# Performance work log

Measured on AMD Instinct MI355X. Metric: run time of the kernel, lower is better.

The kernel has to match this reference:

```python
import jax, jax.numpy as jnp
import numpy as np

B, S, D, H = 2, 2048, 1024, 16
DK = D // H  # 64, per-head key/value dim


def setup_inputs() -> dict:
    key = jax.random.key(0)
    ks = jax.random.split(key, 8)
    q = jax.random.normal(ks[0], (B, S, D), dtype=jnp.float32)
    k = jax.random.normal(ks[1], (B, S, D), dtype=jnp.float32)
    v = jax.random.normal(ks[2], (B, S, D), dtype=jnp.float32)
    # per-head projection weights, initialized like torch.randn in the original
    W_q = jax.random.normal(ks[3], (H, D, DK), dtype=jnp.float32)
    W_k = jax.random.normal(ks[4], (H, D, DK), dtype=jnp.float32)
    W_v = jax.random.normal(ks[5], (H, D, DK), dtype=jnp.float32)
    # output nn.Linear(H*DK, D): weight [D, H*DK], bias [D]
    bound = 1.0 / np.sqrt(H * DK)
    W_o = jax.random.uniform(ks[6], (D, H * DK), dtype=jnp.float32, minval=-bound, maxval=bound)
    b_o = jax.random.uniform(ks[7], (D,), dtype=jnp.float32, minval=-bound, maxval=bound)
    return {"q": q, "k": k, "v": v, "W_q": W_q, "W_k": W_k, "W_v": W_v, "W_o": W_o, "b_o": b_o}


def reference(q, k, v, W_q, W_k, W_v, W_o, b_o):
    dk = W_q.shape[-1]
    # batched per-head projections (replaces the Python loop over heads)
    qh = jnp.einsum('bsd,hdk->bhsk', q, W_q)  # [B,H,S,DK]
    kh = jnp.einsum('bsd,hdk->bhsk', k, W_k)
    vh = jnp.einsum('bsd,hdk->bhsk', v, W_v)
    scale = jnp.asarray(np.sqrt(dk), qh.dtype)
    scores = jnp.einsum('bhsk,bhtk->bhst', qh, kh) / scale  # [B,H,S,S]
    attn = jax.nn.softmax(scores, axis=-1)
    ctx = jnp.einsum('bhst,bhtk->bhsk', attn, vh)  # [B,H,S,DK]
    # concat heads along feature dim (matches torch.cat(..., dim=2))
    b, h, s, d = ctx.shape
    ctx = ctx.transpose(0, 2, 1, 3).reshape(b, s, h * d)  # [B,S,H*DK]
    return ctx @ W_o.T + b_o  # [B,S,D]
```

## Files before the change

kernel.cpp:

```cpp
#include <hip/hip_runtime.h>
#include <math.h>

#define B_ 2
#define S_ 2048
#define D_ 1024
#define H_ 16
#define ATTN_C 0.18033688011f

typedef unsigned short ushort_t;
typedef __attribute__((ext_vector_type(8))) short short8;
typedef __attribute__((ext_vector_type(4))) short short4v;
typedef __attribute__((ext_vector_type(4))) float f32x4;
typedef __attribute__((ext_vector_type(2))) float f32x2;
typedef __attribute__((ext_vector_type(16))) float f32x16;
typedef __attribute__((ext_vector_type(4))) unsigned int uint4v;

#define MFMA(A, B, C) __builtin_amdgcn_mfma_f32_32x32x16_bf16((A), (B), (C), 0, 0, 0)
#define Z16 {0.f,0.f,0.f,0.f,0.f,0.f,0.f,0.f,0.f,0.f,0.f,0.f,0.f,0.f,0.f,0.f}

__device__ __forceinline__ ushort_t bf16rn(float x) {
    unsigned int u = __builtin_bit_cast(unsigned int, x);
    u += 0x7FFFu + ((u >> 16) & 1u);
    return (ushort_t)(u >> 16);
}
__device__ __forceinline__ float bf16tof(ushort_t h) {
    return __builtin_bit_cast(float, (unsigned int)h << 16);
}
__device__ __forceinline__ unsigned cvtpk(float lo, float hi) {
    unsigned r;
    asm("v_cvt_pk_bf16_f32 %0, %1, %2" : "=v"(r) : "v"(lo), "v"(hi));
    return r;
}
__device__ __forceinline__ void gload16(const void* g, void* l) {
    __builtin_amdgcn_global_load_lds(
        (const __attribute__((address_space(1))) unsigned int*)(unsigned long long)g,
        (__attribute__((address_space(3))) unsigned int*)(unsigned int)(unsigned long long)l,
        16, 0, 0);
}

__global__ __launch_bounds__(256) void cvtx_kernel(
    const float* __restrict__ Xq, const float* __restrict__ Xk,
    const float* __restrict__ Xv,
    ushort_t* __restrict__ Xh, ushort_t* __restrict__ Xl)
{
    const int pr = blockIdx.y;
    const float* X = pr == 0 ? Xq : pr == 1 ? Xk : Xv;
    const size_t idx = ((size_t)blockIdx.x * 256 + threadIdx.x) * 8;
    f32x4 v0 = *(const f32x4*)(X + idx);
    f32x4 v1 = *(const f32x4*)(X + idx + 4);
    float f[8] = {v0.x, v0.y, v0.z, v0.w, v1.x, v1.y, v1.z, v1.w};
    short8 hi, lo;
#pragma unroll
    for (int i = 0; i < 8; ++i) {
        ushort_t hh = bf16rn(f[i]);
        hi[i] = (short)hh;
        lo[i] = (short)bf16rn(f[i] - bf16tof(hh));
    }
    const size_t base = (size_t)pr * 2 * S_ * D_;
    *(short8*)(Xh + base + idx) = hi;
    if (pr < 2) *(short8*)(Xl + base + idx) = lo;
}

__global__ __launch_bounds__(256) void cvtw_kernel(
    const float* __restrict__ Wq, const float* __restrict__ Wk,
    const float* __restrict__ Wv,
    ushort_t* __restrict__ wqh, ushort_t* __restrict__ wql,
    ushort_t* __restrict__ wkh, ushort_t* __restrict__ wkl,
    ushort_t* __restrict__ wvh)
{
    __shared__ float T[64][68];
    const int dt = blockIdx.x, h = blockIdx.y, mat = blockIdx.z;
    const int tid = threadIdx.x;
    const float* W = mat == 0 ? Wq : mat == 1 ? Wk : Wv;
    const float* Wb = W + ((size_t)h * 1024 + dt * 64) * 64;
#pragma unroll
    for (int u = 0; u < 4; ++u) {
        int idx = tid + u * 256;
        int d = idx >> 4, c4 = idx & 15;
        f32x4 v = *(const f32x4*)(Wb + (size_t)d * 64 + c4 * 4);
        T[d][c4 * 4 + 0] = v.x; T[d][c4 * 4 + 1] = v.y;
        T[d][c4 * 4 + 2] = v.z; T[d][c4 * 4 + 3] = v.w;
    }
    __syncthreads();
    ushort_t* oh = mat == 0 ? wqh : mat == 1 ? wkh : wvh;
    ushort_t* ol = mat == 0 ? wql : mat == 1 ? wkl : nullptr;
#pragma unroll
    for (int u = 0; u < 4; ++u) {
        int idx = tid + u * 256;
        int n = idx >> 4, c4 = idx & 15;
        float v0 = T[c4 * 4 + 0][n], v1 = T[c4 * 4 + 1][n];
        float v2 = T[c4 * 4 + 2][n], v3 = T[c4 * 4 + 3][n];
        ushort_t h0 = bf16rn(v0), h1 = bf16rn(v1), h2 = bf16rn(v2), h3 = bf16rn(v3);
        size_t off = ((size_t)h * 64 + n) * 1024 + dt * 64 + c4 * 4;
        short4v hv = {(short)h0, (short)h1, (short)h2, (short)h3};
        *(short4v*)(oh + off) = hv;
        if (ol) {
            short4v lv = {(short)bf16rn(v0 - bf16tof(h0)), (short)bf16rn(v1 - bf16tof(h1)),
                          (short)bf16rn(v2 - bf16tof(h2)), (short)bf16rn(v3 - bf16tof(h3))};
            *(short4v*)(ol + off) = lv;
        }
    }
}

__global__ __launch_bounds__(256) void cvtwo_kernel(
    const float* __restrict__ Wo, ushort_t* __restrict__ wob)
{
    size_t idx = (size_t)blockIdx.x * 256 + threadIdx.x;
    f32x4 v = *(const f32x4*)(Wo + idx * 4);
    short4v o = {(short)bf16rn(v.x), (short)bf16rn(v.y),
                 (short)bf16rn(v.z), (short)bf16rn(v.w)};
    *(short4v*)(wob + idx * 4) = o;
}

__global__ __launch_bounds__(256, 2) void proj_kernel(
    const ushort_t* __restrict__ Xh, const ushort_t* __restrict__ Xl,
    const ushort_t* __restrict__ Wh_q, const ushort_t* __restrict__ Wl_q,
    const ushort_t* __restrict__ Wh_k, const ushort_t* __restrict__ Wl_k,
    const ushort_t* __restrict__ Wh_v,
    ushort_t* __restrict__ Oq_h, ushort_t* __restrict__ Oq_l,
    ushort_t* __restrict__ Ok_h, ushort_t* __restrict__ Ok_l,
    ushort_t* __restrict__ Ovt)
{
    __shared__ __align__(16) ushort_t Xs[128 * 128];
    __shared__ __align__(16) ushort_t Ws[128 * 128];
    const int tid = threadIdx.x;
    const int wv = tid >> 6, lane = tid & 63;
    const int lo32 = lane & 31, g = lane >> 5;
    const int wm = wv >> 1, wn = wv & 1;
    const int lrow = lane >> 4, lg = lane & 15;
    const int m0 = blockIdx.x * 128;
    const int n0 = blockIdx.y * 128;
    const int pr = blockIdx.z >> 1, b = blockIdx.z & 1;
    const bool split = (pr != 2);
    const ushort_t* Whp = pr == 0 ? Wh_q : pr == 1 ? Wh_k : Wh_v;
    const ushort_t* Wlp = pr == 0 ? Wl_q : pr == 1 ? Wl_k : Wh_v;
    const ushort_t* Xhb = Xh + ((size_t)(pr * 2 + b) * S_ + m0) * D_;
    const ushort_t* Xlb = Xl + ((size_t)(pr * 2 + b) * S_ + m0) * D_;
    f32x16 a00 = Z16, a01 = Z16, a10 = Z16, a11 = Z16;

    for (int d0 = 0; d0 < D_; d0 += 64) {
        __syncthreads();
#pragma unroll
        for (int u = 0; u < 8; ++u) {
            int row = u * 16 + wv * 4 + lrow;
            int gs = lg ^ (row & 15);
            int half = gs >> 3, c8 = gs & 7;
            const ushort_t* srcX = ((half && split) ? Xlb : Xhb) + (size_t)row * D_ + d0 + c8 * 8;
            gload16(srcX, (char*)Xs + (u * 16 + wv * 4) * 256);
            const ushort_t* srcW = ((half && split) ? Wlp : Whp) + (size_t)(n0 + row) * 1024 + d0 + c8 * 8;
            gload16(srcW, (char*)Ws + (u * 16 + wv * 4) * 256);
        }
        __syncthreads();
#pragma unroll
        for (int ks = 0; ks < 4; ++ks) {
            int coff = ks * 16 + g * 8;
            int r0 = wm * 64 + lo32, r1 = r0 + 32;
            int c0 = wn * 64 + lo32, c1 = c0 + 32;
            short8 a0h = *(const short8*)&Xs[(r0 * 128 + coff) ^ ((r0 & 15) << 3)];
            short8 a1h = *(const short8*)&Xs[(r1 * 128 + coff) ^ ((r1 & 15) << 3)];
            short8 b0h = *(const short8*)&Ws[(c0 * 128 + coff) ^ ((c0 & 15) << 3)];
            short8 b1h = *(const short8*)&Ws[(c1 * 128 + coff) ^ ((c1 & 15) << 3)];
            a00 = MFMA(a0h, b0h, a00);
            a01 = MFMA(a0h, b1h, a01);
            a10 = MFMA(a1h, b0h, a10);
            a11 = MFMA(a1h, b1h, a11);
            if (split) {
                short8 a0l = *(const short8*)&Xs[(r0 * 128 + 64 + coff) ^ ((r0 & 15) << 3)];
                short8 a1l = *(const short8*)&Xs[(r1 * 128 + 64 + coff) ^ ((r1 & 15) << 3)];
                short8 b0l = *(const short8*)&Ws[(c0 * 128 + 64 + coff) ^ ((c0 & 15) << 3)];
                short8 b1l = *(const short8*)&Ws[(c1 * 128 + 64 + coff) ^ ((c1 & 15) << 3)];
                a00 = MFMA(a0h, b0l, a00); a00 = MFMA(a0l, b0h, a00);
                a01 = MFMA(a0h, b1l, a01); a01 = MFMA(a0l, b1h, a01);
                a10 = MFMA(a1h, b0l, a10); a10 = MFMA(a1l, b0h, a10);
                a11 = MFMA(a1h, b1l, a11); a11 = MFMA(a1l, b1h, a11);
            }
        }
    }
    ushort_t* OH = pr == 0 ? Oq_h : pr == 1 ? Ok_h : Ovt;
    ushort_t* OL = pr == 0 ? Oq_l : pr == 1 ? Ok_l : Ovt;
    const bool qscale = (pr == 0);
#define PROJ_STORE(ACC, MT, NT)                                               \
    _Pragma("unroll")                                                         \
    for (int r = 0; r < 16; ++r) {                                            \
        int s_loc = m0 + wm * 64 + (MT) * 32 + (r & 3) + 8 * (r >> 2) + 4 * g;\
        int col = n0 + wn * 64 + (NT) * 32 + lo32;                            \
        int hh_ = col >> 6, nn = col & 63;                                    \
        float val = ACC[r];                                                   \
        if (qscale) val *= ATTN_C;                                            \
        if (split) {                                                          \
            size_t off = (((size_t)b * H_ + hh_) * S_ + s_loc) * 64 + nn;     \
            ushort_t hv = bf16rn(val);                                        \
            OH[off] = hv;                                                     \
            OL[off] = bf16rn(val - bf16tof(hv));                              \
        } else {                                                              \
            size_t offt = (((size_t)b * H_ + hh_) * 64 + nn) * S_ + s_loc;    \
            OH[offt] = bf16rn(val);                                           \
        }                                                                     \
    }
    PROJ_STORE(a00, 0, 0)
    PROJ_STORE(a01, 0, 1)
    PROJ_STORE(a10, 1, 0)
    PROJ_STORE(a11, 1, 1)
#undef PROJ_STORE
}

__global__ __launch_bounds__(256, 2) void attn_kernel(
    const ushort_t* __restrict__ qh_h, const ushort_t* __restrict__ qh_l,
    const ushort_t* __restrict__ kh_h, const ushort_t* __restrict__ kh_l,
    const ushort_t* __restrict__ vt, ushort_t* __restrict__ Opart,
    float* __restrict__ Ml)
{
    __shared__ __align__(16) char smem[32768];
    ushort_t* Vt = (ushort_t*)smem;
    const int tid = threadIdx.x;
    const int wv = tid >> 6, lane = tid & 63;
    const int lo32 = lane & 31, g = lane >> 5;
    const int lrow = lane >> 4, lg = lane & 15;
    const int s0 = blockIdx.x * 256;
    const int h = blockIdx.y;
    const int b = blockIdx.z >> 1, sp = blockIdx.z & 1;
    const size_t bhs = ((size_t)b * H_ + h) * S_ * 64;

    short8 qfh[2][4], qfl[2][4];
#pragma unroll
    for (int c = 0; c < 2; ++c) {
        const ushort_t* Qrh = qh_h + bhs + (size_t)(s0 + wv * 64 + c * 32 + lo32) * 64;
        const ushort_t* Qrl = qh_l + bhs + (size_t)(s0 + wv * 64 + c * 32 + lo32) * 64;
#pragma unroll
        for (int ks = 0; ks < 4; ++ks) {
            qfh[c][ks] = *(const short8*)(Qrh + ks * 16 + g * 8);
            qfl[c][ks] = *(const short8*)(Qrl + ks * 16 + g * 8);
        }
    }
    const ushort_t* Kgh = kh_h + bhs;
    const ushort_t* Kgl = kh_l + bhs;
    const ushort_t* Vtg = vt + ((size_t)b * H_ + h) * 64 * S_;

    f32x16 o00 = Z16, o01 = Z16, o10 = Z16, o11 = Z16;
    float mrun0 = -3.0e38f, mrun1 = -3.0e38f;
    float lrun0 = 0.f, lrun1 = 0.f;
    const int kvbeg = sp * (S_ / 2);

#define MAX16(ST) fmaxf(fmaxf(fmaxf(fmaxf(ST[0], ST[1]), fmaxf(ST[2], ST[3])),   \
                              fmaxf(fmaxf(ST[4], ST[5]), fmaxf(ST[6], ST[7]))),  \
                        fmaxf(fmaxf(fmaxf(ST[8], ST[9]), fmaxf(ST[10], ST[11])), \
                              fmaxf(fmaxf(ST[12], ST[13]), fmaxf(ST[14], ST[15]))))

#define SOFTMAX_PV(ST, MR, LR, OA, OB)                                        \
    {                                                                         \
        float cme = MAX16(ST);                                                \
        cme = fmaxf(cme, __shfl_xor(cme, 32));                                \
        if (!__all(cme <= MR)) {                                              \
            float mnew = fmaxf(MR, cme);                                      \
            float corr = __builtin_amdgcn_exp2f(MR - mnew);                   \
            LR *= corr;                                                       \
            _Pragma("unroll")                                                 \
            for (int r = 0; r < 16; ++r) { OA[r] *= corr; OB[r] *= corr; }    \
            MR = mnew;                                                        \
        }                                                                     \
        float p[16], ls = 0.f;                                                \
        _Pragma("unroll")                                                     \
        for (int r = 0; r < 16; ++r) {                                        \
            p[r] = __builtin_amdgcn_exp2f(ST[r] - MR);                        \
            ls += p[r];                                                       \
        }                                                                     \
        LR += ls;                                                             \
        {                                                                     \
            unsigned w0 = cvtpk(p[0], p[1]), w1 = cvtpk(p[2], p[3]);          \
            unsigned w2 = cvtpk(p[4], p[5]), w3 = cvtpk(p[6], p[7]);          \
            asm("v_permlane32_swap_b32 %0, %1" : "+v"(w0), "+v"(w2));         \
            asm("v_permlane32_swap_b32 %0, %1" : "+v"(w1), "+v"(w3));         \
            uint4v pa = {w0, w1, w2, w3};                                     \
            short8 pf = __builtin_bit_cast(short8, pa);                       \
            OA = MFMA(vfa0, pf, OA);                                          \
            OB = MFMA(vfa1, pf, OB);                                          \
            w0 = cvtpk(p[8], p[9]);  w1 = cvtpk(p[10], p[11]);                \
            w2 = cvtpk(p[12], p[13]); w3 = cvtpk(p[14], p[15]);               \
            asm("v_permlane32_swap_b32 %0, %1" : "+v"(w0), "+v"(w2));         \
            asm("v_permlane32_swap_b32 %0, %1" : "+v"(w1), "+v"(w3));         \
            uint4v pb = {w0, w1, w2, w3};                                     \
            short8 pf2 = __builtin_bit_cast(short8, pb);                      \
            OA = MFMA(vfb0, pf2, OA);                                         \
            OB = MFMA(vfb1, pf2, OB);                                         \
        }                                                                     \
    }

#define LOADK(CI, DST)                                                        \
    {                                                                         \
        int cc = (CI) > 31 ? 31 : (CI);                                       \
        const ushort_t* pn = Kgh + (size_t)(kvbeg + cc * 32 + lo32) * 64 + g * 8; \
        DST[0] = *(const short8*)(pn);                                        \
        DST[1] = *(const short8*)(pn + 16);                                   \
        DST[2] = *(const short8*)(pn + 32);                                   \
        DST[3] = *(const short8*)(pn + 48);                                   \
    }

#define CHUNK_BODY(KC, KN, CI)                                                \
    {                                                                         \
        LOADK((CI) + 1, KN);                                                  \
        f32x16 st0 = Z16, st1 = Z16;                                          \
        st0 = MFMA(KC[0], qfh[0][0], st0);  st1 = MFMA(KC[0], qfh[1][0], st1);\
        st0 = MFMA(KC[1], qfh[0][1], st0);  st1 = MFMA(KC[1], qfh[1][1], st1);\
        st0 = MFMA(KC[2], qfh[0][2], st0);  st1 = MFMA(KC[2], qfh[1][2], st1);\
        st0 = MFMA(KC[3], qfh[0][3], st0);  st1 = MFMA(KC[3], qfh[1][3], st1);\
        float cm0 = MAX16(st0);                                               \
        float cm1 = MAX16(st1);                                               \
        cm0 = fmaxf(cm0, __shfl_xor(cm0, 32));                                \
        cm1 = fmaxf(cm1, __shfl_xor(cm1, 32));                                \
        const bool need0 = !__all(cm0 <= mrun0 - 150.f);                      \
        const bool need1 = !__all(cm1 <= mrun1 - 150.f);                      \
        if (need0 | need1) {                                                  \
            const ushort_t* pl = Kgl + (size_t)(kvbeg + (CI) * 32 + lo32) * 64 + g * 8; \
            short8 kl0 = *(const short8*)(pl);                                \
            short8 kl1 = *(const short8*)(pl + 16);                           \
            short8 kl2 = *(const short8*)(pl + 32);                           \
            short8 kl3 = *(const short8*)(pl + 48);                           \
            if (need0) {                                                      \
                st0 = MFMA(KC[0], qfl[0][0], st0); st0 = MFMA(KC[1], qfl[0][1], st0); \
                st0 = MFMA(KC[2], qfl[0][2], st0); st0 = MFMA(KC[3], qfl[0][3], st0); \
            }                                                                 \
            if (need1) {                                                      \
                st1 = MFMA(KC[0], qfl[1][0], st1); st1 = MFMA(KC[1], qfl[1][1], st1); \
                st1 = MFMA(KC[2], qfl[1][2], st1); st1 = MFMA(KC[3], qfl[1][3], st1); \
            }                                                                 \
            if (need0) {                                                      \
                st0 = MFMA(kl0, qfh[0][0], st0); st0 = MFMA(kl1, qfh[0][1], st0); \
                st0 = MFMA(kl2, qfh[0][2], st0); st0 = MFMA(kl3, qfh[0][3], st0); \
            }                                                                 \
            if (need1) {                                                      \
                st1 = MFMA(kl0, qfh[1][0], st1); st1 = MFMA(kl1, qfh[1][1], st1); \
                st1 = MFMA(kl2, qfh[1][2], st1); st1 = MFMA(kl3, qfh[1][3], st1); \
            }                                                                 \
            const int kvb = ((CI) & 3) * 32;                                  \
            const int vsw = (lo32 & 7) << 3;                                  \
            short8 vfa0 = *(const short8*)&Vt[(lo32 * 128 + kvb + g * 8) ^ vsw];        \
            short8 vfa1 = *(const short8*)&Vt[((lo32 + 32) * 128 + kvb + g * 8) ^ vsw]; \
            short8 vfb0 = *(const short8*)&Vt[(lo32 * 128 + kvb + 16 + g * 8) ^ vsw];   \
            short8 vfb1 = *(const short8*)&Vt[((lo32 + 32) * 128 + kvb + 16 + g * 8) ^ vsw]; \
            if (need0) SOFTMAX_PV(st0, mrun0, lrun0, o00, o01)                \
            if (need1) SOFTMAX_PV(st1, mrun1, lrun1, o10, o11)                \
        }                                                                     \
    }

    short8 kx[4], ky[4];
    LOADK(0, kx);
    int c = 0;
    for (int t = 0; t < 8; ++t) {
        const int kv0 = kvbeg + t * 128;
        __syncthreads();
#pragma unroll
        for (int u = 0; u < 4; ++u) {
            int d = u * 16 + wv * 4 + lrow;
            int gsrc = (lg & 8) | ((lg & 7) ^ (d & 7));
            const ushort_t* src = Vtg + (size_t)d * S_ + kv0 + gsrc * 8;
            gload16(src, (char*)Vt + (u * 16 + wv * 4) * 256);
        }
        __syncthreads();
        CHUNK_BODY(kx, ky, c + 0)
        CHUNK_BODY(ky, kx, c + 1)
        CHUNK_BODY(kx, ky, c + 2)
        CHUNK_BODY(ky, kx, c + 3)
        c += 4;
    }
#undef CHUNK_BODY
#undef LOADK
#undef SOFTMAX_PV
#undef MAX16

    lrun0 += __shfl_xor(lrun0, 32);
    lrun1 += __shfl_xor(lrun1, 32);
    __syncthreads();
    float* Oe = ((float*)smem) + wv * 2048;
    const size_t orowb = (size_t)sp * (B_ * H_ * S_) + ((size_t)b * H_ + h) * S_ + s0 + wv * 64;
#pragma unroll
    for (int r = 0; r < 16; ++r) {
        int dd = (r & 3) + 8 * (r >> 2) + 4 * g;
        int qsw = (lo32 & 7) << 2;
        Oe[(lo32 * 64 + dd) ^ qsw] = o00[r];
        Oe[(lo32 * 64 + 32 + dd) ^ qsw] = o01[r];
    }
#pragma unroll
    for (int rep = 0; rep < 8; ++rep) {
        int idx = lane + rep * 64;
        int qq = idx >> 4, d4 = idx & 15;
        f32x4 ov = *(const f32x4*)&Oe[(qq * 64 + d4 * 4) ^ ((qq & 7) << 2)];
        short4v pk4 = {(short)bf16rn(ov.x), (short)bf16rn(ov.y),
                       (short)bf16rn(ov.z), (short)bf16rn(ov.w)};
        *(short4v*)(Opart + (orowb + qq) * 64 + d4 * 4) = pk4;
    }
    if (g == 0) {
        f32x2 ml = {mrun0, lrun0};
        *(f32x2*)(Ml + (orowb + lo32) * 2) = ml;
    }
    __builtin_amdgcn_s_waitcnt(0);
#pragma unroll
    for (int r = 0; r < 16; ++r) {
        int dd = (r & 3) + 8 * (r >> 2) + 4 * g;
        int qsw = (lo32 & 7) << 2;
        Oe[(lo32 * 64 + dd) ^ qsw] = o10[r];
        Oe[(lo32 * 64 + 32 + dd) ^ qsw] = o11[r];
    }
#pragma unroll
    for (int rep = 0; rep < 8; ++rep) {
        int idx = lane + rep * 64;
        int qq = idx >> 4, d4 = idx & 15;
        f32x4 ov = *(const f32x4*)&Oe[(qq * 64 + d4 * 4) ^ ((qq & 7) << 2)];
        short4v pk4 = {(short)bf16rn(ov.x), (short)bf16rn(ov.y),
                       (short)bf16rn(ov.z), (short)bf16rn(ov.w)};
        *(short4v*)(Opart + (orowb + 32 + qq) * 64 + d4 * 4) = pk4;
    }
    if (g == 0) {
        f32x2 ml = {mrun1, lrun1};
        *(f32x2*)(Ml + (orowb + 32 + lo32) * 2) = ml;
    }
}

__global__ __launch_bounds__(256) void merge_kernel(
    const ushort_t* __restrict__ Opart, const float* __restrict__ Ml,
    ushort_t* __restrict__ ctxb)
{
    const int NROW = B_ * H_ * S_;
    int gidx = blockIdx.x * 256 + threadIdx.x;
    int row = gidx >> 3, d8 = (gidx & 7) * 8;
    f32x2 ml0 = *(const f32x2*)(Ml + (size_t)row * 2);
    f32x2 ml1 = *(const f32x2*)(Ml + ((size_t)NROW + row) * 2);
    float M = fmaxf(ml0.x, ml1.x);
    float w0 = __builtin_amdgcn_exp2f(ml0.x - M);
    float w1 = __builtin_amdgcn_exp2f(ml1.x - M);
    float inv = 1.f / (ml0.y * w0 + ml1.y * w1);
    w0 *= inv; w1 *= inv;
    short8 a = *(const short8*)(Opart + (size_t)row * 64 + d8);
    short8 c = *(const short8*)(Opart + ((size_t)NROW + row) * 64 + d8);
    short8 o;
#pragma unroll
    for (int i = 0; i < 8; ++i) {
        float f = bf16tof((ushort_t)a[i]) * w0 + bf16tof((ushort_t)c[i]) * w1;
        o[i] = (short)bf16rn(f);
    }
    int bb = row >> 15, hh = (row >> 11) & 15, s = row & 2047;
    *(short8*)(ctxb + ((size_t)bb * S_ + s) * D_ + hh * 64 + d8) = o;
}

__global__ __launch_bounds__(128, 2) void outproj_kernel(
    const ushort_t* __restrict__ ctxb, const ushort_t* __restrict__ wob,
    const float* __restrict__ bo, float* __restrict__ Out)
{
    __shared__ __align__(16) ushort_t Cs[128 * 128];
    __shared__ __align__(16) ushort_t Ws2[64 * 128];
    const int tid = threadIdx.x;
    const int wv = tid >> 6, lane = tid & 63;
    const int lo32 = lane & 31, g = lane >> 5;
    const int lrow = lane >> 4, lg = lane & 15;
    const int n0 = blockIdx.x * 64;
    const int m0 = blockIdx.y * 128;
    f32x16 a00 = Z16, a01 = Z16, a10 = Z16, a11 = Z16;
    for (int k0 = 0; k0 < D_; k0 += 128) {
        __syncthreads();
#pragma unroll
        for (int u = 0; u < 16; ++u) {
            int row = u * 8 + wv * 4 + lrow;
            int gs = lg ^ (row & 15);
            const ushort_t* src = ctxb + (size_t)(m0 + row) * D_ + k0 + gs * 8;
            gload16(src, (char*)Cs + (u * 8 + wv * 4) * 256);
        }
#pragma unroll
        for (int u = 0; u < 8; ++u) {
            int row = u * 8 + wv * 4 + lrow;
            int gs = lg ^ (row & 15);
            const ushort_t* src = wob + (size_t)(n0 + row) * D_ + k0 + gs * 8;
            gload16(src, (char*)Ws2 + (u * 8 + wv * 4) * 256);
        }
        __syncthreads();
#pragma unroll
        for (int ks = 0; ks < 8; ++ks) {
            int coff = ks * 16 + g * 8;
            int r0 = wv * 64 + lo32, r1 = r0 + 32;
            int n1 = lo32 + 32;
            short8 A0 = *(const short8*)&Cs[(r0 * 128 + coff) ^ ((r0 & 15) << 3)];
            short8 A1 = *(const short8*)&Cs[(r1 * 128 + coff) ^ ((r1 & 15) << 3)];
            short8 B0 = *(const short8*)&Ws2[(lo32 * 128 + coff) ^ ((lo32 & 15) << 3)];
            short8 B1 = *(const short8*)&Ws2[(n1 * 128 + coff) ^ ((n1 & 15) << 3)];
            a00 = MFMA(A0, B0, a00);
            a01 = MFMA(A0, B1, a01);
            a10 = MFMA(A1, B0, a10);
            a11 = MFMA(A1, B1, a11);
        }
    }
    float b0v = bo[n0 + lo32], b1v = bo[n0 + 32 + lo32];
#define OUT_STORE(ACC, MT, NT, BV)                                          \
    _Pragma("unroll")                                                       \
    for (int r = 0; r < 16; ++r) {                                          \
        int m = m0 + wv * 64 + (MT) * 32 + (r & 3) + 8 * (r >> 2) + 4 * g;  \
        int n = n0 + (NT) * 32 + lo32;                                      \
        Out[(size_t)m * D_ + n] = ACC[r] + (BV);                            \
    }
    OUT_STORE(a00, 0, 0, b0v)
    OUT_STORE(a01, 0, 1, b1v)
    OUT_STORE(a10, 1, 0, b0v)
    OUT_STORE(a11, 1, 1, b1v)
#undef OUT_STORE
}

extern "C" void kernel_launch(void* const* d_in, const int* in_sizes, int n_in,
                              void* d_out, int out_size, void* d_ws,
                              size_t ws_size, hipStream_t stream)
{
    const float* q = (const float*)d_in[0];
    const float* k = (const float*)d_in[1];
    const float* v = (const float*)d_in[2];
    const float* W_q = (const float*)d_in[3];
    const float* W_k = (const float*)d_in[4];
    const float* W_v = (const float*)d_in[5];
    const float* W_o = (const float*)d_in[6];
    const float* b_o = (const float*)d_in[7];
    float* out = (float*)d_out;

    ushort_t* wqt_h = (ushort_t*)d_ws;
    ushort_t* wqt_l = wqt_h + (1 << 20);
    ushort_t* wkt_h = wqt_l + (1 << 20);
    ushort_t* wkt_l = wkt_h + (1 << 20);
    ushort_t* wvt_h = wkt_l + (1 << 20);
    ushort_t* wob   = wvt_h + (1 << 20);
    ushort_t* qh_h  = wob + (1 << 20);
    ushort_t* qh_l  = qh_h + (1 << 22);
    ushort_t* kh_h  = qh_l + (1 << 22);
    ushort_t* kh_l  = kh_h + (1 << 22);
    ushort_t* vtp   = kh_l + (1 << 22);
    ushort_t* Xh    = vtp + (1 << 22);
    ushort_t* Xl    = Xh + 3 * (1 << 22);
    ushort_t* ctxb  = Xh;
    ushort_t* Opart = Xl;
    float*    Ml    = (float*)(Xl + 2 * (size_t)(B_ * H_ * S_) * 64);

    cvtx_kernel<<<dim3(2048, 3), 256, 0, stream>>>(q, k, v, Xh, Xl);
    cvtw_kernel<<<dim3(16, 16, 3), 256, 0, stream>>>(
        W_q, W_k, W_v, wqt_h, wqt_l, wkt_h, wkt_l, wvt_h);
    cvtwo_kernel<<<1024, 256, 0, stream>>>(W_o, wob);
    proj_kernel<<<dim3(16, 8, 6), 256, 0, stream>>>(
        Xh, Xl, wqt_h, wqt_l, wkt_h, wkt_l, wvt_h,
        qh_h, qh_l, kh_h, kh_l, vtp);
    attn_kernel<<<dim3(8, 16, 4), 256, 0, stream>>>(
        qh_h, qh_l, kh_h, kh_l, vtp, Opart, Ml);
    merge_kernel<<<2048, 256, 0, stream>>>(Opart, Ml, ctxb);
    outproj_kernel<<<dim3(16, 32), 128, 0, stream>>>(ctxb, wob, b_o, out);
}
```

Measured before the change: 232.9 us.

## Always compute split-bf16 QK scores with prefetched K low part and larger V tiles

The attention loop now always runs the three-term bf16 split QK product (hi*hi, lo*hi, hi*lo), with the K low part prefetched alongside the K high part instead of loaded on demand behind a wave-uniform branch. The V tile staged in shared memory doubles from 128 to 256 keys per barrier pair, with a new swizzle and load pattern, halving the number of syncs per block. The skip test becomes a simpler per-chunk __any check with a threshold of 126, and the running max is reused from the already-computed chunk max. This removes dependent load latency and branchy MFMA issue, at the cost of more registers, more MFMA work on chunks that were previously skipped, and a larger shared-memory footprint.

```diff
diff --git a/kernel.cpp b/kernel.cpp
--- a/kernel.cpp
+++ b/kernel.cpp
@@ -215,7 +215,6 @@
     const int tid = threadIdx.x;
     const int wv = tid >> 6, lane = tid & 63;
     const int lo32 = lane & 31, g = lane >> 5;
-    const int lrow = lane >> 4, lg = lane & 15;
     const int s0 = blockIdx.x * 256;
     const int h = blockIdx.y;
     const int b = blockIdx.z >> 1, sp = blockIdx.z & 1;
@@ -246,12 +245,10 @@
                         fmaxf(fmaxf(fmaxf(ST[8], ST[9]), fmaxf(ST[10], ST[11])), \
                               fmaxf(fmaxf(ST[12], ST[13]), fmaxf(ST[14], ST[15]))))
 
-#define SOFTMAX_PV(ST, MR, LR, OA, OB)                                        \
+#define SOFTMAX_PV(ST, CME, MR, LR, OA, OB)                                   \
     {                                                                         \
-        float cme = MAX16(ST);                                                \
-        cme = fmaxf(cme, __shfl_xor(cme, 32));                                \
-        if (!__all(cme <= MR)) {                                              \
-            float mnew = fmaxf(MR, cme);                                      \
+        if (__any(CME > MR)) {                                                \
+            float mnew = fmaxf(MR, CME);                                      \
             float corr = __builtin_amdgcn_exp2f(MR - mnew);                   \
             LR *= corr;                                                       \
             _Pragma("unroll")                                                 \
@@ -285,82 +282,74 @@
         }                                                                     \
     }
 
-#define LOADK(CI, DST)                                                        \
+#define LOADK(CI, DH, DL)                                                     \
     {                                                                         \
         int cc = (CI) > 31 ? 31 : (CI);                                       \
         const ushort_t* pn = Kgh + (size_t)(kvbeg + cc * 32 + lo32) * 64 + g * 8; \
-        DST[0] = *(const short8*)(pn);                                        \
-        DST[1] = *(const short8*)(pn + 16);                                   \
-        DST[2] = *(const short8*)(pn + 32);                                   \
-        DST[3] = *(const short8*)(pn + 48);                                   \
-    }
-
-#define CHUNK_BODY(KC, KN, CI)                                                \
+        DH[0] = *(const short8*)(pn);                                         \
+        DH[1] = *(const short8*)(pn + 16);                                    \
+        DH[2] = *(const short8*)(pn + 32);                                    \
+        DH[3] = *(const short8*)(pn + 48);                                    \
+        const ushort_t* pl = Kgl + (size_t)(kvbeg + cc * 32 + lo32) * 64 + g * 8; \
+        DL[0] = *(const short8*)(pl);                                         \
+        DL[1] = *(const short8*)(pl + 16);                                    \
+        DL[2] = *(const short8*)(pl + 32);                                    \
+        DL[3] = *(const short8*)(pl + 48);                                    \
+    }
+
+#define CHUNK_BODY(KH, KL, KHN, KLN, CI)                                      \
     {                                                                         \
-        LOADK((CI) + 1, KN);                                                  \
+        LOADK((CI) + 1, KHN, KLN);                                            \
         f32x16 st0 = Z16, st1 = Z16;                                          \
-        st0 = MFMA(KC[0], qfh[0][0], st0);  st1 = MFMA(KC[0], qfh[1][0], st1);\
-        st0 = MFMA(KC[1], qfh[0][1], st0);  st1 = MFMA(KC[1], qfh[1][1], st1);\
-        st0 = MFMA(KC[2], qfh[0][2], st0);  st1 = MFMA(KC[2], qfh[1][2], st1);\
-        st0 = MFMA(KC[3], qfh[0][3], st0);  st1 = MFMA(KC[3], qfh[1][3], st1);\
+        st0 = MFMA(KH[0], qfh[0][0], st0); st1 = MFMA(KH[0], qfh[1][0], st1); \
+        st0 = MFMA(KH[1], qfh[0][1], st0); st1 = MFMA(KH[1], qfh[1][1], st1); \
+        st0 = MFMA(KH[2], qfh[0][2], st0); st1 = MFMA(KH[2], qfh[1][2], st1); \
+        st0 = MFMA(KH[3], qfh[0][3], st0); st1 = MFMA(KH[3], qfh[1][3], st1); \
+        st0 = MFMA(KL[0], qfh[0][0], st0); st1 = MFMA(KL[0], qfh[1][0], st1); \
+        st0 = MFMA(KL[1], qfh[0][1], st0); st1 = MFMA(KL[1], qfh[1][1], st1); \
+        st0 = MFMA(KL[2], qfh[0][2], st0); st1 = MFMA(KL[2], qfh[1][2], st1); \
+        st0 = MFMA(KL[3], qfh[0][3], st0); st1 = MFMA(KL[3], qfh[1][3], st1); \
+        st0 = MFMA(KH[0], qfl[0][0], st0); st1 = MFMA(KH[0], qfl[1][0], st1); \
+        st0 = MFMA(KH[1], qfl[0][1], st0); st1 = MFMA(KH[1], qfl[1][1], st1); \
+        st0 = MFMA(KH[2], qfl[0][2], st0); st1 = MFMA(KH[2], qfl[1][2], st1); \
+        st0 = MFMA(KH[3], qfl[0][3], st0); st1 = MFMA(KH[3], qfl[1][3], st1); \
+        const int kvb = ((CI) & 7) * 32;                                      \
+        const int vsw = (lo32 & 15) << 3;                                     \
         float cm0 = MAX16(st0);                                               \
         float cm1 = MAX16(st1);                                               \
         cm0 = fmaxf(cm0, __shfl_xor(cm0, 32));                                \
         cm1 = fmaxf(cm1, __shfl_xor(cm1, 32));                                \
-        const bool need0 = !__all(cm0 <= mrun0 - 150.f);                      \
-        const bool need1 = !__all(cm1 <= mrun1 - 150.f);                      \
-        if (need0 | need1) {                                                  \
-            const ushort_t* pl = Kgl + (size_t)(kvbeg + (CI) * 32 + lo32) * 64 + g * 8; \
-            short8 kl0 = *(const short8*)(pl);                                \
-            short8 kl1 = *(const short8*)(pl + 16);                           \
-            short8 kl2 = *(const short8*)(pl + 32);                           \
-            short8 kl3 = *(const short8*)(pl + 48);                           \
-            if (need0) {                                                      \
-                st0 = MFMA(KC[0], qfl[0][0], st0); st0 = MFMA(KC[1], qfl[0][1], st0); \
-                st0 = MFMA(KC[2], qfl[0][2], st0); st0 = MFMA(KC[3], qfl[0][3], st0); \
-            }                                                                 \
-            if (need1) {                                                      \
-                st1 = MFMA(KC[0], qfl[1][0], st1); st1 = MFMA(KC[1], qfl[1][1], st1); \
-                st1 = MFMA(KC[2], qfl[1][2], st1); st1 = MFMA(KC[3], qfl[1][3], st1); \
-            }                                                                 \
-            if (need0) {                                                      \
-                st0 = MFMA(kl0, qfh[0][0], st0); st0 = MFMA(kl1, qfh[0][1], st0); \
-                st0 = MFMA(kl2, qfh[0][2], st0); st0 = MFMA(kl3, qfh[0][3], st0); \
-            }                                                                 \
-            if (need1) {                                                      \
-                st1 = MFMA(kl0, qfh[1][0], st1); st1 = MFMA(kl1, qfh[1][1], st1); \
-                st1 = MFMA(kl2, qfh[1][2], st1); st1 = MFMA(kl3, qfh[1][3], st1); \
-            }                                                                 \
-            const int kvb = ((CI) & 3) * 32;                                  \
-            const int vsw = (lo32 & 7) << 3;                                  \
-            short8 vfa0 = *(const short8*)&Vt[(lo32 * 128 + kvb + g * 8) ^ vsw];        \
-            short8 vfa1 = *(const short8*)&Vt[((lo32 + 32) * 128 + kvb + g * 8) ^ vsw]; \
-            short8 vfb0 = *(const short8*)&Vt[(lo32 * 128 + kvb + 16 + g * 8) ^ vsw];   \
-            short8 vfb1 = *(const short8*)&Vt[((lo32 + 32) * 128 + kvb + 16 + g * 8) ^ vsw]; \
-            if (need0) SOFTMAX_PV(st0, mrun0, lrun0, o00, o01)                \
-            if (need1) SOFTMAX_PV(st1, mrun1, lrun1, o10, o11)                \
-        }                                                                     \
-    }
-
-    short8 kx[4], ky[4];
-    LOADK(0, kx);
+        short8 vfa0 = *(const short8*)&Vt[(lo32 * 256 + kvb + g * 8) ^ vsw];        \
+        short8 vfa1 = *(const short8*)&Vt[((lo32 + 32) * 256 + kvb + g * 8) ^ vsw]; \
+        short8 vfb0 = *(const short8*)&Vt[(lo32 * 256 + kvb + 16 + g * 8) ^ vsw];   \
+        short8 vfb1 = *(const short8*)&Vt[((lo32 + 32) * 256 + kvb + 16 + g * 8) ^ vsw]; \
+        if (__any(cm0 > mrun0 - 126.f)) SOFTMAX_PV(st0, cm0, mrun0, lrun0, o00, o01) \
+        if (__any(cm1 > mrun1 - 126.f)) SOFTMAX_PV(st1, cm1, mrun1, lrun1, o10, o11) \
+    }
+
+    short8 ka_h[4], ka_l[4], kb_h[4], kb_l[4];
+    LOADK(0, ka_h, ka_l);
     int c = 0;
-    for (int t = 0; t < 8; ++t) {
-        const int kv0 = kvbeg + t * 128;
+    for (int t = 0; t < 4; ++t) {
+        const int kv0 = kvbeg + t * 256;
         __syncthreads();
 #pragma unroll
-        for (int u = 0; u < 4; ++u) {
-            int d = u * 16 + wv * 4 + lrow;
-            int gsrc = (lg & 8) | ((lg & 7) ^ (d & 7));
-            const ushort_t* src = Vtg + (size_t)d * S_ + kv0 + gsrc * 8;
-            gload16(src, (char*)Vt + (u * 16 + wv * 4) * 256);
+        for (int u = 0; u < 8; ++u) {
+            int rowb = u * 8 + wv * 2;
+            int d = rowb + (lane >> 5);
+            const ushort_t* src = Vtg + (size_t)d * S_ + kv0 + 8 * ((lane & 31) ^ (d & 15));
+            gload16(src, (char*)Vt + rowb * 512);
         }
         __syncthreads();
-        CHUNK_BODY(kx, ky, c + 0)
-        CHUNK_BODY(ky, kx, c + 1)
-        CHUNK_BODY(kx, ky, c + 2)
-        CHUNK_BODY(ky, kx, c + 3)
-        c += 4;
+        CHUNK_BODY(ka_h, ka_l, kb_h, kb_l, c + 0)
+        CHUNK_BODY(kb_h, kb_l, ka_h, ka_l, c + 1)
+        CHUNK_BODY(ka_h, ka_l, kb_h, kb_l, c + 2)
+        CHUNK_BODY(kb_h, kb_l, ka_h, ka_l, c + 3)
+        CHUNK_BODY(ka_h, ka_l, kb_h, kb_l, c + 4)
+        CHUNK_BODY(kb_h, kb_l, ka_h, ka_l, c + 5)
+        CHUNK_BODY(ka_h, ka_l, kb_h, kb_l, c + 6)
+        CHUNK_BODY(kb_h, kb_l, ka_h, ka_l, c + 7)
+        c += 8;
     }
 #undef CHUNK_BODY
 #undef LOADK
```

Measured after the change: 269.1 us. +15.5%, slower.
